# Kernel optimization log

Measured on AMD Instinct MI355X. Metric: run time of the kernel, lower is better.

The kernel has to match this reference:

```python
import jax, jax.numpy as jnp
import numpy as np

N_ANCHORS = 250000
IMG_H, IMG_W = 1024, 1024
PRE_NMS = 6000    # num_pre_nms_test (inference path, training=False)
POST_NMS = 300    # num_post_nms_test
IOU_THR = 0.7


def setup_inputs() -> dict:
    key = jax.random.key(0)
    k1, k2, k3, k4, k5 = jax.random.split(key, 5)
    bboxes_txtytwth = jax.random.normal(k1, (N_ANCHORS, 4), dtype=jnp.float32) * 0.1
    # anchors as (ymin, xmin, ymax, xmax) scattered over the image
    cy = jax.random.uniform(k2, (N_ANCHORS,), dtype=jnp.float32) * IMG_H
    cx = jax.random.uniform(k3, (N_ANCHORS,), dtype=jnp.float32) * IMG_W
    ah = 32.0 + jax.random.uniform(k4, (N_ANCHORS,), dtype=jnp.float32) * 224.0
    aw = 32.0 + jax.random.uniform(k5, (N_ANCHORS,), dtype=jnp.float32) * 224.0
    anchors = jnp.stack([cy - 0.5 * ah, cx - 0.5 * aw,
                         cy + 0.5 * ah, cx + 0.5 * aw], axis=1)
    scores = jax.random.normal(jax.random.fold_in(key, 7), (N_ANCHORS,), dtype=jnp.float32)
    return {
        "bboxes_txtytwth": bboxes_txtytwth,
        "anchors": anchors,
        "scores": scores,
        "image_height": IMG_H,
        "image_width": IMG_W,
        "extractor_stride": 16,
    }


def _decode_bbox(anchors, deltas):
    # anchors: [N,4] (ymin,xmin,ymax,xmax); deltas: [N,4] (ty,tx,th,tw)
    h = anchors[:, 2] - anchors[:, 0]
    w = anchors[:, 3] - anchors[:, 1]
    cy = anchors[:, 0] + 0.5 * h
    cx = anchors[:, 1] + 0.5 * w
    ty, tx, th, tw = deltas[:, 0], deltas[:, 1], deltas[:, 2], deltas[:, 3]
    ncy = ty * h + cy
    ncx = tx * w + cx
    nh = jnp.exp(th) * h
    nw = jnp.exp(tw) * w
    return jnp.stack([ncy - 0.5 * nh, ncx - 0.5 * nw,
                      ncy + 0.5 * nh, ncx + 0.5 * nw], axis=1)


def _iou_matrix(b):
    # b: [K,4] -> [K,K] pairwise IoU
    area = (b[:, 2] - b[:, 0]) * (b[:, 3] - b[:, 1])
    iy = jnp.maximum(0.0, jnp.minimum(b[:, None, 2], b[None, :, 2]) -
                     jnp.maximum(b[:, None, 0], b[None, :, 0]))
    ix = jnp.maximum(0.0, jnp.minimum(b[:, None, 3], b[None, :, 3]) -
                     jnp.maximum(b[:, None, 1], b[None, :, 1]))
    inter = iy * ix
    return inter / (area[:, None] + area[None, :] - inter + 1e-9)


def _rpn_proposal(bboxes_txtytwth, anchors, scores, image_height, image_width,
                  extractor_stride):
    # 1) decode
    boxes = _decode_bbox(anchors, bboxes_txtytwth)
    # 2) clip to image + min-edge filter (filter implemented as score mask)
    ymin = jnp.clip(boxes[:, 0], 0.0, image_height)
    xmin = jnp.clip(boxes[:, 1], 0.0, image_width)
    ymax = jnp.clip(boxes[:, 2], 0.0, image_height)
    xmax = jnp.clip(boxes[:, 3], 0.0, image_width)
    boxes = jnp.stack([ymin, xmin, ymax, xmax], axis=1)
    valid = ((ymax - ymin) >= extractor_stride) & ((xmax - xmin) >= extractor_stride)
    masked_scores = jnp.where(valid, scores, -jnp.inf)
    # 3) pre-NMS top-k (sorted descending by score)
    top_scores, top_idx = jax.lax.top_k(masked_scores, PRE_NMS)
    top_boxes = boxes[top_idx]                      # [PRE_NMS,4]
    valid_k = jnp.isfinite(top_scores)
    # 4) greedy NMS over score-sorted boxes
    iou = _iou_matrix(top_boxes)                    # [PRE_NMS, PRE_NMS]
    order = jnp.arange(PRE_NMS)

    def body(i, suppressed):
        alive_i = jnp.logical_not(suppressed[i]) & valid_k[i]
        return suppressed | (alive_i & (iou[i] > IOU_THR) & (order > i))

    suppressed = jax.lax.fori_loop(0, PRE_NMS, body,
                                   jnp.zeros((PRE_NMS,), dtype=bool))
    keep = jnp.logical_not(suppressed) & valid_k
    # 5) first POST_NMS kept boxes (already score-ordered), fixed-shape output
    rank = jnp.cumsum(keep) - 1                     # position among kept
    tgt = jnp.where(keep & (rank < POST_NMS), rank, POST_NMS)
    out = jnp.zeros((POST_NMS + 1, 4), dtype=top_boxes.dtype).at[tgt].set(top_boxes)
    return out[:POST_NMS]                           # [POST_NMS,4], zero-padded


def reference(bboxes_txtytwth, anchors, scores, image_height, image_width,
              extractor_stride):
    return _rpn_proposal(bboxes_txtytwth, anchors, scores,
                         float(image_height), float(image_width),
                         float(extractor_stride))
```

## Files before the change

### kernel.cpp

```cpp
#include <hip/hip_runtime.h>

#pragma clang fp contract(off)

#define N_PRE   6000
#define N_POST  300
#define NW      94
#define SELCAP  7936
#define RS_BLK  124
#define NBIN    16384
#define DSHIFT  18
#define HPART   64

struct SelState {
    unsigned int thr;
};

static __device__ __forceinline__ unsigned long long readlane64(unsigned long long v, int l) {
    unsigned lo = __builtin_amdgcn_readlane((unsigned)v, l);
    unsigned hi = __builtin_amdgcn_readlane((unsigned)(v >> 32), l);
    return ((unsigned long long)hi << 32) | lo;
}

__global__ void decode_kernel(const float4* __restrict__ deltas,
                              const float4* __restrict__ anchors,
                              const float*  __restrict__ scores,
                              const int* __restrict__ ph, const int* __restrict__ pw,
                              const int* __restrict__ ps,
                              unsigned int* __restrict__ s32out,
                              float4* __restrict__ boxes,
                              unsigned long long* __restrict__ sel,
                              unsigned long long* __restrict__ valid_words,
                              unsigned int* __restrict__ counter, int N)
{
#pragma clang fp contract(off)
    if (blockIdx.x == 0) {
        for (int t = threadIdx.x; t < SELCAP; t += 256) sel[t] = 0ull;
    } else if (blockIdx.x == 1) {
        if (threadIdx.x < 128) valid_words[threadIdx.x] = 0ull;
        if (threadIdx.x == 0) *counter = 0u;
    }
    int i = blockIdx.x * blockDim.x + threadIdx.x;
    if (i >= N) return;
    float H = (float)(*ph), W = (float)(*pw), S = (float)(*ps);
    float4 d = deltas[i];
    float4 a = anchors[i];
    float h = a.z - a.x, w = a.w - a.y;
    float cy = a.x + 0.5f * h, cx = a.y + 0.5f * w;
    float ncy = d.x * h + cy;
    float ncx = d.y * w + cx;
    float eh = (float)exp((double)d.z);
    float ew = (float)exp((double)d.w);
    float nh = eh * h;
    float nw = ew * w;
    float ymin = ncy - 0.5f * nh, xmin = ncx - 0.5f * nw;
    float ymax = ncy + 0.5f * nh, xmax = ncx + 0.5f * nw;
    ymin = fminf(fmaxf(ymin, 0.0f), H);
    xmin = fminf(fmaxf(xmin, 0.0f), W);
    ymax = fminf(fmaxf(ymax, 0.0f), H);
    xmax = fminf(fmaxf(xmax, 0.0f), W);
    bool valid = (ymax - ymin >= S) && (xmax - xmin >= S);
    float sc = scores[i];
    unsigned int bits = __float_as_uint(sc);
    unsigned int s32;
    if (!valid) s32 = 0x007FFFFFu;
    else        s32 = (bits & 0x80000000u) ? ~bits : (bits | 0x80000000u);
    s32out[i] = s32;
    boxes[i]  = make_float4(ymin, xmin, ymax, xmax);
}

__global__ __launch_bounds__(256) void hist_part(const unsigned int* __restrict__ s32in,
                                                 unsigned int* __restrict__ phist, int N)
{
    __shared__ unsigned int lh[NBIN];
    int tid = threadIdx.x;
    for (int j = tid; j < NBIN; j += 256) lh[j] = 0u;
    __syncthreads();
    for (int i = blockIdx.x * 256 + tid; i < N; i += HPART * 256)
        atomicAdd(&lh[s32in[i] >> DSHIFT], 1u);
    __syncthreads();
    unsigned int* dst = phist + blockIdx.x * NBIN;
    for (int j = tid; j < NBIN; j += 256) dst[j] = lh[j];
}

__global__ __launch_bounds__(256) void hist_reduce(const unsigned int* __restrict__ phist,
                                                   unsigned int* __restrict__ hist)
{
    int j = blockIdx.x * 256 + threadIdx.x;
    unsigned int s = 0;
#pragma unroll 8
    for (int b = 0; b < HPART; b++) s += phist[b * NBIN + j];
    hist[j] = s;
}

__global__ __launch_bounds__(1024) void pick_pass(const unsigned int* __restrict__ hist,
                                                  SelState* __restrict__ state)
{
    __shared__ unsigned int wsum[16];
    __shared__ int sel_chunk;
    __shared__ unsigned int sel_above;
    int tid = threadIdx.x, lane = tid & 63, wave = tid >> 6;
    const unsigned int k = 6000u;

    unsigned int s = 0;
    int base = tid * 16;
#pragma unroll
    for (int i = 0; i < 16; i++) s += hist[base + i];
    unsigned int S = s;
    for (int d = 1; d < 64; d <<= 1) {
        unsigned int t = __shfl_down(S, d);
        if (lane + d < 64) S += t;
    }
    if (lane == 0) wsum[wave] = S;
    __syncthreads();
    unsigned int above = 0;
    for (int w2 = wave + 1; w2 < 16; w2++) above += wsum[w2];
    unsigned int F  = S + above;
    unsigned int Fn = F - s;
    if (Fn < k && k <= F) { sel_chunk = tid; sel_above = Fn; }
    __syncthreads();
    int c = sel_chunk;
    unsigned int acc = sel_above;
    if (wave == 0 && lane < 16) {
        unsigned int b = hist[c * 16 + lane];
        unsigned int B = b;
        for (int d = 1; d < 16; d <<= 1) {
            unsigned int t = __shfl_down(B, d);
            if (lane + d < 16) B += t;
        }
        unsigned int Bn = B - b;
        unsigned int kk = k - acc;
        if (Bn < kk && kk <= B) state->thr = (unsigned int)(c * 16 + lane);
    }
}

__global__ void compact_kernel(const unsigned int* __restrict__ s32in,
                               const SelState* __restrict__ state,
                               unsigned long long* __restrict__ sel,
                               unsigned int* __restrict__ counter, int N)
{
    int i = blockIdx.x * blockDim.x + threadIdx.x;
    if (i >= N) return;
    unsigned int s32 = s32in[i];
    if ((s32 >> DSHIFT) >= state->thr) {
        unsigned int p = atomicAdd(counter, 1u);
        if (p < SELCAP)
            sel[p] = ((unsigned long long)s32 << 32) |
                     (unsigned long long)(~(unsigned int)i);
    }
}

__global__ __launch_bounds__(1024) void rank_scatter(
    const unsigned long long* __restrict__ sel,
    const float4* __restrict__ boxes,
    float4* __restrict__ boxes_sorted,
    unsigned long long* __restrict__ valid_words, int N)
{
    __shared__ __align__(16) unsigned long long kbuf[SELCAP];
    __shared__ unsigned int cnt[64];
    int tid = threadIdx.x;
    if (tid < 64) cnt[tid] = 0u;
    for (int t = tid; t < SELCAP; t += 1024) kbuf[t] = sel[t];
    __syncthreads();
    int lane = tid & 63;
    int slice = tid >> 6;
    int i = blockIdx.x * 64 + lane;
    unsigned long long my = kbuf[i];
    const int SL = SELCAP / 16;
    int j0 = slice * SL;
    unsigned int c = 0;
#pragma unroll 8
    for (int j = j0; j < j0 + SL; j += 2) {
        ulonglong2 kk = *reinterpret_cast<const ulonglong2*>(&kbuf[j]);
        c += (kk.x > my) || (kk.x == my && j < i);
        c += (kk.y > my) || (kk.y == my && (j + 1) < i);
    }
    atomicAdd(&cnt[lane], c);
    __syncthreads();
    if (tid < 64) {
        unsigned int rank = cnt[tid];
        unsigned long long key = kbuf[blockIdx.x * 64 + tid];
        if (key != 0ull && rank < N_PRE) {
            unsigned int s32 = (unsigned int)(key >> 32);
            unsigned int ii  = ~(unsigned int)(key & 0xFFFFFFFFull);
            float4 b = (ii < (unsigned int)N) ? boxes[ii] : make_float4(0.f,0.f,0.f,0.f);
            boxes_sorted[rank] = b;
            bool v = (s32 != 0x007FFFFFu) && (ii < (unsigned int)N);
            if (v) atomicOr(&valid_words[rank >> 6], 1ull << (rank & 63));
        }
    }
}

__global__ __launch_bounds__(64) void mask_kernel(const float4* __restrict__ boxes_sorted,
                                                  unsigned long long* __restrict__ mask,
                                                  unsigned long long* __restrict__ diagT,
                                                  unsigned long long* __restrict__ bandT)
{
#pragma clang fp contract(off)
    int rb = blockIdx.y, cb = blockIdx.x;
    if (cb < rb) return;
    __shared__ float4 cbox[64];
    int tid = threadIdx.x;
    int col0 = cb * 64;
    int c = col0 + tid;
    cbox[tid] = (c < N_PRE) ? boxes_sorted[c] : make_float4(0.f, 0.f, 0.f, 0.f);
    __syncthreads();
    int i = rb * 64 + tid;
    if (i >= N_PRE) return;
    float4 bi = boxes_sorted[i];
    float area_i = (bi.z - bi.x) * (bi.w - bi.y);
    unsigned long long word = 0ull;
#pragma unroll 8
    for (int j = 0; j < 64; j++) {
        float4 bj = cbox[j];
        float iy = fminf(bi.z, bj.z) - fmaxf(bi.x, bj.x);
        iy = fmaxf(iy, 0.0f);
        float ix = fminf(bi.w, bj.w) - fmaxf(bi.y, bj.y);
        ix = fmaxf(ix, 0.0f);
        float inter = iy * ix;
        float area_j = (bj.z - bj.x) * (bj.w - bj.y);
        float iou = inter / (((area_i + area_j) - inter) + 1e-9f);
        if ((col0 + j) > i && iou > 0.7f) word |= (1ull << j);
    }
    mask[(size_t)i * NW + cb] = word;

    if (cb == rb || cb == rb + 1) {
        unsigned long long colw = 0ull;
        for (int jj = 0; jj < 64; jj++) {
            unsigned long long t = __ballot((unsigned int)((word >> jj) & 1ull));
            if (tid == jj) colw = t;
        }
        if (cb == rb) diagT[rb * 64 + tid] = colw;
        else          bandT[rb * 64 + tid] = colw;
    }
}

__global__ __launch_bounds__(64) void nms_seq(const unsigned long long* __restrict__ mask,
                                              const unsigned long long* __restrict__ diagT,
                                              const unsigned long long* __restrict__ bandT,
                                              const unsigned long long* __restrict__ valid_words,
                                              const float4* __restrict__ boxes_sorted,
                                              float* __restrict__ out)
{
#pragma clang fp contract(off)
    int lane = threadIdx.x;
    float4* out4 = reinterpret_cast<float4*>(out);

    for (int t = lane; t < N_POST; t += 64)
        out4[t] = make_float4(0.f, 0.f, 0.f, 0.f);

    unsigned long long vw0 = valid_words[lane];
    unsigned long long vw1 = (lane < NW - 64) ? valid_words[64 + lane] : 0ull;
    unsigned long long rem0 = ~vw0;
    unsigned long long rem1 = ~vw1;

    unsigned long long pA_lo[8] = {0,0,0,0,0,0,0,0}, pA_hi[8] = {0,0,0,0,0,0,0,0};
    unsigned long long pB_lo[8] = {0,0,0,0,0,0,0,0}, pB_hi[8] = {0,0,0,0,0,0,0,0};

    unsigned long long carryword = 0ull;
    int rank = 0;

    unsigned long long dT = diagT[lane];
    unsigned long long bT = bandT[lane];
    float4 cb = boxes_sorted[lane];

#define WORD_STEP(WV, PLO, PHI)                                                 \
    {                                                                           \
        int w = (WV);                                                           \
               \
        rem0 |= ((PLO[0]|PLO[1])|(PLO[2]|PLO[3]))|((PLO[4]|PLO[5])|(PLO[6]|PLO[7])); \
        rem1 |= ((PHI[0]|PHI[1])|(PHI[2]|PHI[3]))|((PHI[4]|PHI[5])|(PHI[6]|PHI[7])); \
               \
        unsigned long long dTn = 0ull, bTn = 0ull;                              \
        float4 cbn = cb;                                                        \
        if (w + 1 < NW) {                                                       \
            dTn = diagT[(w + 1) * 64 + lane];                                   \
            bTn = bandT[(w + 1) * 64 + lane];                                   \
            cbn = boxes_sorted[(w + 1) * 64 + lane];                            \
        }                                                                       \
        unsigned long long remw = (w < 64) ? readlane64(rem0, w)                \
                                           : readlane64(rem1, w - 64);          \
        unsigned long long vw   = (w < 64) ? readlane64(vw0, w)                 \
                                           : readlane64(vw1, w - 64);           \
        unsigned long long alive = vw & ~remw & ~carryword;                     \
        unsigned int carryacc = 0u;                                             \
        unsigned long long keptb = 0ull;                                        \
        while (alive) {                                                         \
            int b = __builtin_ctzll(alive);                   \
            unsigned int supme = (unsigned int)((dT >> b) & 1ull);              \
            carryacc |= (unsigned int)((bT >> b) & 1ull);                       \
            if (lane == b) out4[rank] = cb;                                     \
            keptb |= 1ull << b;                                                 \
            rank++;                                                             \
            if (rank >= N_POST) break;                                          \
            unsigned long long supw = __ballot(supme);                          \
            alive &= ~(supw | (1ull << b));                                     \
        }                                                                       \
        if (rank >= N_POST) break;                                              \
        carryword = __ballot(carryacc);                                         \
                     \
        {                                                                       \
            int kc = __popcll(keptb);                                           \
            unsigned long long kb = keptb;                                      \
            _Pragma("unroll")                                                   \
            for (int sslot = 0; sslot < 8; sslot++) {                           \
                if (sslot < kc) {                                               \
                    int bb = __builtin_ctzll(kb); kb &= kb - 1ull;              \
                    const unsigned long long* rp = mask + (size_t)(w * 64 + bb) * NW; \
                    PLO[sslot] = rp[lane];                                      \
                    PHI[sslot] = (lane < NW - 64) ? rp[64 + lane] : 0ull;       \
                } else { PLO[sslot] = 0ull; PHI[sslot] = 0ull; }                \
            }                                                                   \
            while (kb) {            \
                int bb = __builtin_ctzll(kb); kb &= kb - 1ull;                  \
                const unsigned long long* rp = mask + (size_t)(w * 64 + bb) * NW; \
                rem0 |= rp[lane];                                               \
                if (lane < NW - 64) rem1 |= rp[64 + lane];                      \
            }                                                                   \
        }                                                                       \
        dT = dTn; bT = bTn; cb = cbn;                                           \
    }

    for (int w2 = 0; w2 < NW; w2 += 2) {
        WORD_STEP(w2,     pA_lo, pA_hi)
        WORD_STEP(w2 + 1, pB_lo, pB_hi)
    }
#undef WORD_STEP
}

extern "C" void kernel_launch(void* const* d_in, const int* in_sizes, int n_in,
                              void* d_out, int out_size, void* d_ws, size_t ws_size,
                              hipStream_t stream)
{
    const float4* deltas  = (const float4*)d_in[0];
    const float4* anchors = (const float4*)d_in[1];
    const float*  scores  = (const float*)d_in[2];
    const int* ph = (const int*)d_in[3];
    const int* pw = (const int*)d_in[4];
    const int* ps = (const int*)d_in[5];
    int N = in_sizes[2];

    char* base = (char*)d_ws;
    size_t off = 0;
    auto alloc = [&](size_t sz) -> void* {
        void* p = base + off;
        off = (off + sz + 255) & ~(size_t)255;
        return p;
    };
    unsigned int* s32buf = (unsigned int*)alloc(sizeof(unsigned int) * (size_t)N);
    float4* boxes = (float4*)alloc(sizeof(float4) * (size_t)N);
    unsigned int* phist = (unsigned int*)alloc((size_t)HPART * NBIN * sizeof(unsigned int));
    unsigned int* hist = (unsigned int*)alloc(NBIN * sizeof(unsigned int));
    SelState* state = (SelState*)alloc(256);
    unsigned int* counter = (unsigned int*)alloc(256);
    unsigned long long* valid_words = (unsigned long long*)alloc(128 * 8);
    unsigned long long* sel = (unsigned long long*)alloc(sizeof(unsigned long long) * SELCAP);
    float4* boxes_sorted = (float4*)alloc(sizeof(float4) * 6016);
    unsigned long long* diagT = (unsigned long long*)alloc(sizeof(unsigned long long) * NW * 64);
    unsigned long long* bandT = (unsigned long long*)alloc(sizeof(unsigned long long) * NW * 64);
    unsigned long long* mask = (unsigned long long*)alloc(sizeof(unsigned long long) * ((size_t)N_PRE * NW + 32));

    int nb = (N + 255) / 256;
    decode_kernel<<<nb, 256, 0, stream>>>(deltas, anchors, scores, ph, pw, ps,
                                          s32buf, boxes, sel, valid_words, counter, N);
    hist_part<<<HPART, 256, 0, stream>>>(s32buf, phist, N);
    hist_reduce<<<NBIN / 256, 256, 0, stream>>>(phist, hist);
    pick_pass<<<1, 1024, 0, stream>>>(hist, state);
    compact_kernel<<<nb, 256, 0, stream>>>(s32buf, state, sel, counter, N);
    rank_scatter<<<RS_BLK, 1024, 0, stream>>>(sel, boxes, boxes_sorted, valid_words, N);
    mask_kernel<<<dim3(NW, NW), 64, 0, stream>>>(boxes_sorted, mask, diagT, bandT);
    nms_seq<<<1, 64, 0, stream>>>(mask, diagT, bandT, valid_words, boxes_sorted, (float*)d_out);
}
```

Measured before the change: 263.4 us.

## Interleave diag/band masks, defer output writes, shrink prefetch slots in NMS

Merges the diagT and bandT arrays into one interleaved buffer so the sequential NMS loop fetches both with a single 16-byte load per word. It drops the per-word box prefetch and in-loop output store. Instead each lane records the sorted indices of the kept boxes it owns, and all output boxes are gathered once after the loop. The mask-row prefetch slots shrink from 8 to 4 to cut register pressure, and the interleaved buffer is now zeroed in the decode kernel. The aim is to shorten the latency-bound single-wave critical path, at the cost of more fallback non-prefetched row loads when many boxes survive in one word.

```diff
diff --git a/kernel.cpp b/kernel.cpp
--- a/kernel.cpp
+++ b/kernel.cpp
@@ -30,7 +30,8 @@
                               float4* __restrict__ boxes,
                               unsigned long long* __restrict__ sel,
                               unsigned long long* __restrict__ valid_words,
-                              unsigned int* __restrict__ counter, int N)
+                              unsigned int* __restrict__ counter,
+                              unsigned long long* __restrict__ dbT, int N)
 {
 #pragma clang fp contract(off)
     if (blockIdx.x == 0) {
@@ -38,6 +39,9 @@
     } else if (blockIdx.x == 1) {
         if (threadIdx.x < 128) valid_words[threadIdx.x] = 0ull;
         if (threadIdx.x == 0) *counter = 0u;
+    } else if (blockIdx.x == 2 || blockIdx.x == 3) {
+        int base = (blockIdx.x - 2) * (NW * 64);
+        for (int t = threadIdx.x; t < NW * 64; t += 256) dbT[base + t] = 0ull;
     }
     int i = blockIdx.x * blockDim.x + threadIdx.x;
     if (i >= N) return;
@@ -192,8 +196,7 @@
 
 __global__ __launch_bounds__(64) void mask_kernel(const float4* __restrict__ boxes_sorted,
                                                   unsigned long long* __restrict__ mask,
-                                                  unsigned long long* __restrict__ diagT,
-                                                  unsigned long long* __restrict__ bandT)
+                                                  unsigned long long* __restrict__ dbT)
 {
 #pragma clang fp contract(off)
     int rb = blockIdx.y, cb = blockIdx.x;
@@ -229,17 +232,17 @@
             unsigned long long t = __ballot((unsigned int)((word >> jj) & 1ull));
             if (tid == jj) colw = t;
         }
-        if (cb == rb) diagT[rb * 64 + tid] = colw;
-        else          bandT[rb * 64 + tid] = colw;
-    }
-}
-
-__global__ __launch_bounds__(64) void nms_seq(const unsigned long long* __restrict__ mask,
-                                              const unsigned long long* __restrict__ diagT,
-                                              const unsigned long long* __restrict__ bandT,
-                                              const unsigned long long* __restrict__ valid_words,
-                                              const float4* __restrict__ boxes_sorted,
-                                              float* __restrict__ out)
+        if (cb == rb) dbT[2 * (rb * 64 + tid) + 0] = colw;
+        else          dbT[2 * (rb * 64 + tid) + 1] = colw;
+    }
+}
+
+__global__ __launch_bounds__(64, 1) void nms_seq(
+    const unsigned long long* __restrict__ mask,
+    const unsigned long long* __restrict__ dbT,
+    const unsigned long long* __restrict__ valid_words,
+    const float4* __restrict__ boxes_sorted,
+    float* __restrict__ out)
 {
 #pragma clang fp contract(off)
     int lane = threadIdx.x;
@@ -253,29 +256,29 @@
     unsigned long long rem0 = ~vw0;
     unsigned long long rem1 = ~vw1;
 
-    unsigned long long pA_lo[8] = {0,0,0,0,0,0,0,0}, pA_hi[8] = {0,0,0,0,0,0,0,0};
-    unsigned long long pB_lo[8] = {0,0,0,0,0,0,0,0}, pB_hi[8] = {0,0,0,0,0,0,0,0};
+    unsigned long long pA_lo[4] = {0,0,0,0}, pA_hi[4] = {0,0,0,0};
+    unsigned long long pB_lo[4] = {0,0,0,0}, pB_hi[4] = {0,0,0,0};
+
+    int k0 = -1, k1 = -1, k2 = -1, k3 = -1, k4 = -1;
 
     unsigned long long carryword = 0ull;
     int rank = 0;
 
-    unsigned long long dT = diagT[lane];
-    unsigned long long bT = bandT[lane];
-    float4 cb = boxes_sorted[lane];
+    ulonglong2 db = *reinterpret_cast<const ulonglong2*>(&dbT[2 * (0 * 64 + lane)]);
+    unsigned long long dT = db.x, bT = db.y;
 
 #define WORD_STEP(WV, PLO, PHI)                                                 \
     {                                                                           \
         int w = (WV);                                                           \
                \
-        rem0 |= ((PLO[0]|PLO[1])|(PLO[2]|PLO[3]))|((PLO[4]|PLO[5])|(PLO[6]|PLO[7])); \
-        rem1 |= ((PHI[0]|PHI[1])|(PHI[2]|PHI[3]))|((PHI[4]|PHI[5])|(PHI[6]|PHI[7])); \
-               \
+        rem0 |= (PLO[0] | PLO[1]) | (PLO[2] | PLO[3]);                          \
+        rem1 |= (PHI[0] | PHI[1]) | (PHI[2] | PHI[3]);                          \
+            \
         unsigned long long dTn = 0ull, bTn = 0ull;                              \
-        float4 cbn = cb;                                                        \
         if (w + 1 < NW) {                                                       \
-            dTn = diagT[(w + 1) * 64 + lane];                                   \
-            bTn = bandT[(w + 1) * 64 + lane];                                   \
-            cbn = boxes_sorted[(w + 1) * 64 + lane];                            \
+            ulonglong2 dbn = *reinterpret_cast<const ulonglong2*>(              \
+                &dbT[2 * ((w + 1) * 64 + lane)]);                               \
+            dTn = dbn.x; bTn = dbn.y;                                           \
         }                                                                       \
         unsigned long long remw = (w < 64) ? readlane64(rem0, w)                \
                                            : readlane64(rem1, w - 64);          \
@@ -288,8 +291,17 @@
             int b = __builtin_ctzll(alive);                   \
             unsigned int supme = (unsigned int)((dT >> b) & 1ull);              \
             carryacc |= (unsigned int)((bT >> b) & 1ull);                       \
-            if (lane == b) out4[rank] = cb;                                     \
             keptb |= 1ull << b;                                                 \
+            if ((rank & 63) == lane) {                                          \
+                int idx = w * 64 + b;                                           \
+                switch (rank >> 6) {                                            \
+                    case 0: k0 = idx; break;                                    \
+                    case 1: k1 = idx; break;                                    \
+                    case 2: k2 = idx; break;                                    \
+                    case 3: k3 = idx; break;                                    \
+                    default: k4 = idx; break;                                   \
+                }                                                               \
+            }                                                                   \
             rank++;                                                             \
             if (rank >= N_POST) break;                                          \
             unsigned long long supw = __ballot(supme);                          \
@@ -297,12 +309,12 @@
         }                                                                       \
         if (rank >= N_POST) break;                                              \
         carryword = __ballot(carryacc);                                         \
-                     \
+           \
         {                                                                       \
             int kc = __popcll(keptb);                                           \
             unsigned long long kb = keptb;                                      \
             _Pragma("unroll")                                                   \
-            for (int sslot = 0; sslot < 8; sslot++) {                           \
+            for (int sslot = 0; sslot < 4; sslot++) {                           \
                 if (sslot < kc) {                                               \
                     int bb = __builtin_ctzll(kb); kb &= kb - 1ull;              \
                     const unsigned long long* rp = mask + (size_t)(w * 64 + bb) * NW; \
@@ -317,7 +329,7 @@
                 if (lane < NW - 64) rem1 |= rp[64 + lane];                      \
             }                                                                   \
         }                                                                       \
-        dT = dTn; bT = bTn; cb = cbn;                                           \
+        dT = dTn; bT = bTn;                                                     \
     }
 
     for (int w2 = 0; w2 < NW; w2 += 2) {
@@ -325,6 +337,12 @@
         WORD_STEP(w2 + 1, pB_lo, pB_hi)
     }
 #undef WORD_STEP
+
+    if (k0 >= 0) out4[0 * 64 + lane] = boxes_sorted[k0];
+    if (k1 >= 0) out4[1 * 64 + lane] = boxes_sorted[k1];
+    if (k2 >= 0) out4[2 * 64 + lane] = boxes_sorted[k2];
+    if (k3 >= 0) out4[3 * 64 + lane] = boxes_sorted[k3];
+    if (k4 >= 0 && (4 * 64 + lane) < N_POST) out4[4 * 64 + lane] = boxes_sorted[k4];
 }
 
 extern "C" void kernel_launch(void* const* d_in, const int* in_sizes, int n_in,
@@ -355,18 +373,17 @@
     unsigned long long* valid_words = (unsigned long long*)alloc(128 * 8);
     unsigned long long* sel = (unsigned long long*)alloc(sizeof(unsigned long long) * SELCAP);
     float4* boxes_sorted = (float4*)alloc(sizeof(float4) * 6016);
-    unsigned long long* diagT = (unsigned long long*)alloc(sizeof(unsigned long long) * NW * 64);
-    unsigned long long* bandT = (unsigned long long*)alloc(sizeof(unsigned long long) * NW * 64);
+    unsigned long long* dbT = (unsigned long long*)alloc(sizeof(unsigned long long) * NW * 64 * 2);
     unsigned long long* mask = (unsigned long long*)alloc(sizeof(unsigned long long) * ((size_t)N_PRE * NW + 32));
 
     int nb = (N + 255) / 256;
     decode_kernel<<<nb, 256, 0, stream>>>(deltas, anchors, scores, ph, pw, ps,
-                                          s32buf, boxes, sel, valid_words, counter, N);
+                                          s32buf, boxes, sel, valid_words, counter, dbT, N);
     hist_part<<<HPART, 256, 0, stream>>>(s32buf, phist, N);
     hist_reduce<<<NBIN / 256, 256, 0, stream>>>(phist, hist);
     pick_pass<<<1, 1024, 0, stream>>>(hist, state);
     compact_kernel<<<nb, 256, 0, stream>>>(s32buf, state, sel, counter, N);
     rank_scatter<<<RS_BLK, 1024, 0, stream>>>(sel, boxes, boxes_sorted, valid_words, N);
-    mask_kernel<<<dim3(NW, NW), 64, 0, stream>>>(boxes_sorted, mask, diagT, bandT);
-    nms_seq<<<1, 64, 0, stream>>>(mask, diagT, bandT, valid_words, boxes_sorted, (float*)d_out);
-}
+    mask_kernel<<<dim3(NW, NW), 64, 0, stream>>>(boxes_sorted, mask, dbT);
+    nms_seq<<<1, 64, 0, stream>>>(mask, dbT, valid_words, boxes_sorted, (float*)d_out);
+}
```

Measured after the change: 292.9 us. +11.2%, slower.
